# Performance work log

Measured on AMD Instinct MI355X. Metric: run time of the kernel, lower is better.

Reference implementation:

```python
import jax, jax.numpy as jnp
import numpy as np

# dims
N, E, C, HH, HEADS, A, V, D, AE, FH, MAXEL = 10000, 80000, 64, 128, 8, 32, 16, 64, 32, 128, 100
L, K = 2, 9  # lmax=2 -> (L+1)^2 = 9 steerable coefficients
EXPAND = jnp.array([0, 1, 1, 1, 2, 2, 2, 2, 2])          # coeff -> degree l
EXP1 = jnp.array([0, 0, 0, 1, 1, 1, 1, 1])                # coeffs 1..8 -> l-1
L_ONEHOT = jax.nn.one_hot(EXPAND, 3, dtype=jnp.float32)   # [9,3]
COUNTS = jnp.array([1 * C, 3 * C, 5 * C], dtype=jnp.float32)


def so3_linear(h, W, b):
    # per-degree linear (SO3_LinearV2): W [3,Cin,Cout], bias only on l=0
    out = jnp.einsum('nkc,kcd->nkd', h, W[EXPAND])
    return out.at[:, 0].add(b)


def enorm(h):
    # equivariant norm: per-node, per-degree RMS over (m, channels)
    sq = jnp.einsum('nkc,kl->nl', h * h, L_ONEHOT)        # [N,3] sum of squares per l
    scale = jax.lax.rsqrt(sq / COUNTS + 1e-6)             # [N,3]
    return h * scale[:, EXPAND][:, :, None]


def seg_softmax(logits, seg, n):
    m = jax.ops.segment_max(logits, seg, num_segments=n)
    m = jnp.where(jnp.isfinite(m), m, 0.0)
    e = jnp.exp(logits - m[seg])
    s = jax.ops.segment_sum(e, seg, num_segments=n)
    return e / (s[seg] + 1e-9)


def smooth_leaky_relu(z, a=0.2):
    return a * z + (1.0 - a) * z * jax.nn.sigmoid(z)


def setup_inputs():
    key = jax.random.key(0)
    ks = jax.random.split(key, 20)
    p = lambda i, sh, s=0.05: jax.random.normal(ks[i], sh, jnp.float32) * s
    return {
        'x': jax.random.normal(ks[0], (N, K, C), jnp.float32),
        'edge_distance': jax.random.uniform(ks[1], (E, D), dtype=jnp.float32),
        'rl_ij': jax.random.normal(ks[2], (E, K - 1), jnp.float32),
        'src_emb': p(3, (MAXEL, AE), 0.001),
        'tgt_emb': p(4, (MAXEL, AE), 0.001),
        'W1': p(5, (D + 2 * AE, 128)), 'b1': jnp.zeros((128,), jnp.float32),
        'W2': p(6, (128, 3 * 2 * C)), 'b2': jnp.zeros((3 * 2 * C,), jnp.float32),
        'W_conv1': p(7, (3, 2 * C, HH)),
        'W_m0': p(8, (2 * C, HEADS * A + HH + 2 * L * HH)),
        'ln_g': jnp.ones((A,), jnp.float32), 'ln_b': jnp.zeros((A,), jnp.float32),
        'alpha_dot': p(9, (HEADS, A), 0.2),
        'W_xj': p(10, (C, HH)),
        'W_conv2': p(11, (3, HH, HEADS * V)),
        'W_proj': p(12, (3, HEADS * V, C)), 'b_proj': jnp.zeros((C,), jnp.float32),
        'W_gate': p(13, (C, FH)), 'b_gate': jnp.zeros((FH,), jnp.float32),
        'W_ffn1': p(14, (3, C, FH)), 'b_ffn1': jnp.zeros((FH,), jnp.float32),
        'W_ffn2': p(15, (3, FH, C)), 'b_ffn2': jnp.zeros((C,), jnp.float32),
        'atomic_numbers': jax.random.randint(ks[16], (N,), 0, MAXEL),
        'edge_index': jax.random.randint(ks[17], (2, E), 0, N),
    }


def _block(x, edge_distance, rl_ij, src_emb, tgt_emb, W1, b1, W2, b2, W_conv1,
           W_m0, ln_g, ln_b, alpha_dot, W_xj, W_conv2, W_proj, b_proj,
           W_gate, b_gate, W_ffn1, b_ffn1, W_ffn2, b_ffn2,
           atomic_numbers, edge_index):
    src, tgt = edge_index[0], edge_index[1]
    # ---- attention branch (pre-norm) ----
    xn = enorm(x)
    xs, xt = xn[src], xn[tgt]                                    # [E,9,C] gathers
    x_edge = jnp.concatenate([xs, xt], axis=-1)                  # [E,9,2C]
    # radial function with source/target atom embeddings (use_m_share_rad)
    ef = jnp.concatenate([edge_distance, src_emb[atomic_numbers[src]],
                          tgt_emb[atomic_numbers[tgt]]], axis=-1)
    rad = jax.nn.silu(ef @ W1 + b1) @ W2 + b2                    # [E, 3*2C]
    rad = rad.reshape(E, 3, 2 * C)[:, EXPAND]                    # [E,9,2C]
    x_edge = x_edge * rad
    # so2_conv_1: per-degree linear + extra m0 scalar outputs
    msg = jnp.einsum('ekc,kcd->ekd', x_edge, W_conv1[EXPAND])    # [E,9,HH]
    extra = x_edge[:, 0] @ W_m0                                  # [E,896]
    alpha_f = extra[:, :HEADS * A].reshape(E, HEADS, A)
    g_scalar = extra[:, HEADS * A:HEADS * A + HH]                # [E,HH]
    gates = extra[:, HEADS * A + HH:].reshape(E, 2, L, HH)
    g_dir = jax.nn.sigmoid(gates[:, 0])[:, EXP1]                 # [E,8,HH]
    g_ten = jax.nn.sigmoid(gates[:, 1])[:, EXP1]                 # [E,8,HH]
    # GATA value activation: scalar silu + gated direction/tensor terms (l>=1)
    xj_proj = jnp.einsum('ekc,cd->ekd', xs, W_xj)                # [E,9,HH]
    val0 = jax.nn.silu(g_scalar)                                 # [E,HH]
    val_rest = msg[:, 1:] + rl_ij[:, :, None] * g_dir + xj_proj[:, 1:] * g_ten
    val = jnp.concatenate([val0[:, None], val_rest], axis=1)     # [E,9,HH]
    # so2_conv_2
    vout = jnp.einsum('ekd,kdh->ekh', val, W_conv2[EXPAND])      # [E,9,H*V]
    # attention weights
    mu = jnp.mean(alpha_f, axis=-1, keepdims=True)
    var = jnp.var(alpha_f, axis=-1, keepdims=True)
    an = (alpha_f - mu) * jax.lax.rsqrt(var + 1e-5) * ln_g + ln_b
    logits = jnp.einsum('eha,ha->eh', smooth_leaky_relu(an), alpha_dot)
    attn = seg_softmax(logits, tgt, N)                           # [E,HEADS]
    vout = vout.reshape(E, K, HEADS, V) * attn[:, None, :, None]
    node_out = jax.ops.segment_sum(vout.reshape(E, K, HEADS * V), tgt,
                                   num_segments=N)               # [N,9,H*V]
    x = x + so3_linear(node_out, W_proj, b_proj)
    # ---- FFN branch (pre-norm, separable S2-style gating) ----
    yn = enorm(x)
    g = yn[:, 0] @ W_gate + b_gate                               # [N,FH]
    h = so3_linear(yn, W_ffn1, b_ffn1)                           # [N,9,FH]
    h = jnp.concatenate([jax.nn.silu(g)[:, None],
                         h[:, 1:] * jax.nn.sigmoid(g)[:, None, :]], axis=1)
    return x + so3_linear(h, W_ffn2, b_ffn2)


def reference(x, edge_distance, rl_ij, src_emb, tgt_emb, W1, b1, W2, b2,
              W_conv1, W_m0, ln_g, ln_b, alpha_dot, W_xj, W_conv2, W_proj,
              b_proj, W_gate, b_gate, W_ffn1, b_ffn1, W_ffn2, b_ffn2,
              atomic_numbers, edge_index):
    return _block(x, edge_distance, rl_ij, src_emb, tgt_emb, W1, b1, W2, b2,
                  W_conv1, W_m0, ln_g, ln_b, alpha_dot, W_xj, W_conv2, W_proj,
                  b_proj, W_gate, b_gate, W_ffn1, b_ffn1, W_ffn2, b_ffn2,
                  atomic_numbers, edge_index)
```

## Files before the change

### kernel.cpp

```cpp
#include <hip/hip_runtime.h>

#define NN 10000
#define EE 80000

__device__ __forceinline__ float bf2f(unsigned short u) {
  return __uint_as_float(((unsigned)u) << 16);
}
__device__ __forceinline__ unsigned short f2bf(float f) {
  unsigned u = __float_as_uint(f);
  return (unsigned short)((u + 0x7FFFu + ((u >> 16) & 1u)) >> 16);
}
__device__ __forceinline__ float sigm(float x) { return 1.0f / (1.0f + __expf(-x)); }
__device__ __forceinline__ float siluf(float x) { return x * sigm(x); }

__device__ __forceinline__ float ld1(const void* p, long i, bool isf) {
  return isf ? ((const float*)p)[i] : bf2f(((const unsigned short*)p)[i]);
}
__device__ __forceinline__ void st1(void* p, long i, float v, bool isf) {
  if (isf) ((float*)p)[i] = v;
  else     ((unsigned short*)p)[i] = f2bf(v);
}
struct F8 { float v[8]; };
__device__ __forceinline__ F8 ld8(const void* p, long i, bool isf) {
  F8 r;
  if (isf) {
    const float* q = (const float*)p + i;
    float4 a = *(const float4*)q;
    float4 b = *(const float4*)(q + 4);
    r.v[0] = a.x; r.v[1] = a.y; r.v[2] = a.z; r.v[3] = a.w;
    r.v[4] = b.x; r.v[5] = b.y; r.v[6] = b.z; r.v[7] = b.w;
  } else {
    uint4 u = *(const uint4*)((const unsigned short*)p + i);
    r.v[0] = __uint_as_float(u.x << 16); r.v[1] = __uint_as_float(u.x & 0xFFFF0000u);
    r.v[2] = __uint_as_float(u.y << 16); r.v[3] = __uint_as_float(u.y & 0xFFFF0000u);
    r.v[4] = __uint_as_float(u.z << 16); r.v[5] = __uint_as_float(u.z & 0xFFFF0000u);
    r.v[6] = __uint_as_float(u.w << 16); r.v[7] = __uint_as_float(u.w & 0xFFFF0000u);
  }
  return r;
}
__device__ __forceinline__ void ld4v(const void* p, long i, bool isf, float o[4]) {
  if (isf) {
    float4 v = *(const float4*)((const float*)p + i);
    o[0] = v.x; o[1] = v.y; o[2] = v.z; o[3] = v.w;
  } else {
    uint2 u = *(const uint2*)((const unsigned short*)p + i);
    o[0] = bf2f((unsigned short)u.x); o[1] = bf2f((unsigned short)(u.x >> 16));
    o[2] = bf2f((unsigned short)u.y); o[3] = bf2f((unsigned short)(u.y >> 16));
  }
}
__device__ __forceinline__ void ldx4(const unsigned short* p, long i, float o[4]) {
  uint2 u = *(const uint2*)(p + i);
  o[0] = bf2f((unsigned short)u.x); o[1] = bf2f((unsigned short)(u.x >> 16));
  o[2] = bf2f((unsigned short)u.y); o[3] = bf2f((unsigned short)(u.y >> 16));
}
__device__ __forceinline__ void st4bf(unsigned short* dst, float a, float b,
                                      float c, float d) {
  uint2 u;
  u.x = (unsigned)f2bf(a) | ((unsigned)f2bf(b) << 16);
  u.y = (unsigned)f2bf(c) | ((unsigned)f2bf(d) << 16);
  *(uint2*)dst = u;
}
__device__ __forceinline__ float u8f(unsigned v) {
  return (float)(v & 0xFFu) * (1.f / 255.f);
}

typedef __attribute__((ext_vector_type(8))) short bf8v;
typedef __attribute__((ext_vector_type(4))) float f4v;
struct AF128 { bf8v a[4]; };
struct AF64  { bf8v a[2]; };
struct BF128 { bf8v b[4]; };
struct BF64  { bf8v b[2]; };

__device__ __forceinline__ AF128 load_af128(const unsigned short* sA, int pitch, int lane) {
  AF128 f;
  const unsigned short* p = sA + (lane & 15) * pitch + ((lane >> 4) << 3);
#pragma unroll
  for (int kb = 0; kb < 4; ++kb) f.a[kb] = *(const bf8v*)(p + kb * 32);
  return f;
}
__device__ __forceinline__ AF64 load_af64(const unsigned short* sA, int pitch, int lane) {
  AF64 f;
  const unsigned short* p = sA + (lane & 15) * pitch + ((lane >> 4) << 3);
#pragma unroll
  for (int kb = 0; kb < 2; ++kb) f.a[kb] = *(const bf8v*)(p + kb * 32);
  return f;
}
__device__ __forceinline__ BF128 load_b128(const unsigned short* Wt, int row0, int lane) {
  BF128 f;
  const unsigned short* p = Wt + (long)(row0 + (lane & 15)) * 128 + ((lane >> 4) << 3);
#pragma unroll
  for (int kb = 0; kb < 4; ++kb) f.b[kb] = *(const bf8v*)(p + kb * 32);
  return f;
}
__device__ __forceinline__ BF64 load_b64f(const unsigned short* Wt, int row0, int lane) {
  BF64 f;
  const unsigned short* p = Wt + (long)(row0 + (lane & 15)) * 64 + ((lane >> 4) << 3);
#pragma unroll
  for (int kb = 0; kb < 2; ++kb) f.b[kb] = *(const bf8v*)(p + kb * 32);
  return f;
}
__device__ __forceinline__ f4v mfma128f(const AF128& a, const BF128& w) {
  f4v acc = {0.f, 0.f, 0.f, 0.f};
#pragma unroll
  for (int kb = 0; kb < 4; ++kb)
    acc = __builtin_amdgcn_mfma_f32_16x16x32_bf16(a.a[kb], w.b[kb], acc, 0, 0, 0);
  return acc;
}
__device__ __forceinline__ f4v mfma64f(const AF64& a, const BF64& w) {
  f4v acc = {0.f, 0.f, 0.f, 0.f};
#pragma unroll
  for (int kb = 0; kb < 2; ++kb)
    acc = __builtin_amdgcn_mfma_f32_16x16x32_bf16(a.a[kb], w.b[kb], acc, 0, 0, 0);
  return acc;
}
__device__ __forceinline__ f4v mfma128w(const BF128& w, const AF128& x) {
  f4v acc = {0.f, 0.f, 0.f, 0.f};
#pragma unroll
  for (int kb = 0; kb < 4; ++kb)
    acc = __builtin_amdgcn_mfma_f32_16x16x32_bf16(w.b[kb], x.a[kb], acc, 0, 0, 0);
  return acc;
}
__device__ __forceinline__ f4v mfma64w(const BF64& w, const AF64& x) {
  f4v acc = {0.f, 0.f, 0.f, 0.f};
#pragma unroll
  for (int kb = 0; kb < 2; ++kb)
    acc = __builtin_amdgcn_mfma_f32_16x16x32_bf16(w.b[kb], x.a[kb], acc, 0, 0, 0);
  return acc;
}
__device__ __forceinline__ f4v mfma128(const AF128& f, const unsigned short* Wt,
                                       int row0, int lane) {
  return mfma128f(f, load_b128(Wt, row0, lane));
}
__device__ __forceinline__ f4v mfma64(const AF64& f, const unsigned short* Wt,
                                      int row0, int lane) {
  return mfma64f(f, load_b64f(Wt, row0, lane));
}
__device__ __forceinline__ void store8(unsigned short* dst, const unsigned short v[8]) {
  uint4 u;
  u.x = (unsigned)v[0] | ((unsigned)v[1] << 16);
  u.y = (unsigned)v[2] | ((unsigned)v[3] << 16);
  u.z = (unsigned)v[4] | ((unsigned)v[5] << 16);
  u.w = (unsigned)v[6] | ((unsigned)v[7] << 16);
  *(uint4*)dst = u;
}

#define OFF_W1 0
#define OFF_W2 16384
#define OFF_M0 65536
#define OFF_C1 180224
#define OFF_XJ 229376
#define OFF_C2 237568
#define OFF_PJ 286720
#define OFF_G  311296
#define OFF_F1 319488
#define OFF_F2 344064
#define WT_TOTAL 368640

#define WS_SBUF   1177280
#define WS_LOGB   1497280
#define WS_CURS   2777280
#define WS_PERM   2817280
#define WS_NOUT   3137280
#define WS_XN     49217280

__global__ __launch_bounds__(256) void k_repack(
    const void* __restrict__ W1, const void* __restrict__ W2,
    const void* __restrict__ W_m0, const void* __restrict__ W_conv1,
    const void* __restrict__ W_xj, const void* __restrict__ W_conv2,
    const void* __restrict__ W_proj, const void* __restrict__ W_gate,
    const void* __restrict__ W_ffn1, const void* __restrict__ W_ffn2,
    const void* __restrict__ ln_g, unsigned short* __restrict__ wt) {
  const bool isf = (((const unsigned*)ln_g)[0] == 0x3F800000u);
  int i = blockIdx.x * 256 + threadIdx.x;
  float v;
  if (i < 16384)       { int n = i >> 7, k = i & 127; v = ld1(W1, (long)k * 128 + n, isf); }
  else if (i < 65536)  { int j = i - 16384; int n = j >> 7, k = j & 127;
                         v = ld1(W2, (long)k * 384 + n, isf); }
  else if (i < 180224) { int j = i - 65536; int n = j >> 7, k = j & 127;
                         v = ld1(W_m0, (long)k * 896 + n, isf); }
  else if (i < 229376) { int j = i - 180224; int l = j >> 14, r = j & 16383;
                         int n = r >> 7, k = r & 127;
                         v = ld1(W_conv1, (long)(l * 128 + k) * 128 + n, isf); }
  else if (i < 237568) { int j = i - 229376; int n = j >> 6, k = j & 63;
                         v = ld1(W_xj, (long)k * 128 + n, isf); }
  else if (i < 286720) { int j = i - 237568; int l = j >> 14, r = j & 16383;
                         int n = r >> 7, k = r & 127;
                         v = ld1(W_conv2, (long)(l * 128 + k) * 128 + n, isf); }
  else if (i < 311296) { int j = i - 286720; int l = j >> 13, r = j & 8191;
                         int n = r >> 7, k = r & 127;
                         v = ld1(W_proj, (long)(l * 128 + k) * 64 + n, isf); }
  else if (i < 319488) { int j = i - 311296; int n = j >> 6, k = j & 63;
                         v = ld1(W_gate, (long)k * 128 + n, isf); }
  else if (i < 344064) { int j = i - 319488; int l = j >> 13, r = j & 8191;
                         int n = r >> 6, k = r & 63;
                         v = ld1(W_ffn1, (long)(l * 64 + k) * 128 + n, isf); }
  else                 { int j = i - 344064; int l = j >> 13, r = j & 8191;
                         int n = r >> 7, k = r & 127;
                         v = ld1(W_ffn2, (long)(l * 128 + k) * 64 + n, isf); }
  wt[i] = f2bf(v);
}

__global__ __launch_bounds__(256) void k_scales(const void* __restrict__ x,
                                                const void* __restrict__ ln_g,
                                                unsigned short* __restrict__ xn) {
  const bool isf = (((const unsigned*)ln_g)[0] == 0x3F800000u);
  const int n = blockIdx.x * 4 + (threadIdx.x >> 6);
  const int c = threadIdx.x & 63;
  long xb = (long)n * 576;
  float v[9];
#pragma unroll
  for (int k = 0; k < 9; ++k) v[k] = ld1(x, xb + k * 64 + c, isf);
  float q0 = v[0] * v[0], q1 = 0.f, q2 = 0.f;
#pragma unroll
  for (int k = 1; k < 4; ++k) q1 += v[k] * v[k];
#pragma unroll
  for (int k = 4; k < 9; ++k) q2 += v[k] * v[k];
#pragma unroll
  for (int off = 32; off > 0; off >>= 1) {
    q0 += __shfl_xor(q0, off); q1 += __shfl_xor(q1, off); q2 += __shfl_xor(q2, off);
  }
  float s0 = rsqrtf(q0 * (1.f / 64.f)  + 1e-6f);
  float s1 = rsqrtf(q1 * (1.f / 192.f) + 1e-6f);
  float s2 = rsqrtf(q2 * (1.f / 320.f) + 1e-6f);
  xn[xb + c] = f2bf(v[0] * s0);
#pragma unroll
  for (int k = 1; k < 4; ++k) xn[xb + k * 64 + c] = f2bf(v[k] * s1);
#pragma unroll
  for (int k = 4; k < 9; ++k) xn[xb + k * 64 + c] = f2bf(v[k] * s2);
}

__global__ void k_init0(float* __restrict__ p) {
  int i = blockIdx.x * 256 + threadIdx.x;
  if (i < 80000) p[i] = 0.f;
}
__global__ void k_initn(float4* __restrict__ p) {
  int i = blockIdx.x * 256 + threadIdx.x;
  p[i] = make_float4(0.f, 0.f, 0.f, 0.f);
}
__global__ void k_zc(int* __restrict__ c) {
  int i = blockIdx.x * 256 + threadIdx.x;
  if (i < NN) c[i] = 0;
}
__global__ void k_hist(const int* __restrict__ edge_index, int* __restrict__ cnt) {
  int e = blockIdx.x * 256 + threadIdx.x;
  if (e < EE) atomicAdd(&cnt[edge_index[EE + e]], 1);
}
__global__ __launch_bounds__(256) void k_prefix(int* __restrict__ cur) {
  __shared__ int part[256], off0[256];
  const int th = threadIdx.x;
  int cnt[40]; int s = 0;
#pragma unroll 1
  for (int i = 0; i < 40; ++i) {
    int n = th * 40 + i;
    cnt[i] = (n < NN) ? cur[n] : 0;
    s += cnt[i];
  }
  part[th] = s;
  __syncthreads();
  if (th == 0) {
    int acc = 0;
    for (int i = 0; i < 256; ++i) { off0[i] = acc; acc += part[i]; }
  }
  __syncthreads();
  int acc = off0[th];
#pragma unroll 1
  for (int i = 0; i < 40; ++i) {
    int n = th * 40 + i;
    if (n < NN) { cur[n] = acc; acc += cnt[i]; }
  }
}
__global__ void k_scatter(const int* __restrict__ edge_index, int* __restrict__ cur,
                          int* __restrict__ perm) {
  int e = blockIdx.x * 256 + threadIdx.x;
  if (e < EE) {
    int tg = edge_index[EE + e];
    int pos = atomicAdd(&cur[tg], 1);
    perm[pos] = e;
  }
}

__global__ __launch_bounds__(256) void k_logits_e(
    const unsigned short* __restrict__ xn, const void* __restrict__ dist,
    const void* __restrict__ src_emb, const void* __restrict__ tgt_emb,
    const void* __restrict__ b1, const void* __restrict__ b2,
    const void* __restrict__ ln_g, const void* __restrict__ ln_b,
    const void* __restrict__ alpha_dot,
    const int* __restrict__ an, const int* __restrict__ edge_index,
    const unsigned short* __restrict__ wt,
    unsigned short* __restrict__ logitsb, float* __restrict__ sbuf) {
  const bool isf = (((const unsigned*)ln_g)[0] == 0x3F800000u);
  __shared__ int s_src[32], s_tgt[32], s_as[32], s_at[32];
  __shared__ __align__(16) unsigned short sA[32 * 136];
  __shared__ __align__(16) unsigned short sA2[32 * 136];
  __shared__ __align__(16) unsigned short sFB[32 * 264];

  const int t = threadIdx.x;
  int bid = blockIdx.x;
  int x8 = bid & 7, i8 = bid >> 3;
  int wg = (x8 < 4 ? x8 * 313 : 1252 + (x8 - 4) * 312) + i8;
  const int e0 = wg * 32;
  const int lane = t & 63, wave = t >> 6, lm = lane & 15, lq = lane >> 4;

  if (t < 32) {
    int eid = e0 + t;
    int s = edge_index[eid], g = edge_index[EE + eid];
    s_src[t] = s; s_tgt[t] = g;
    s_as[t] = an[s]; s_at[t] = an[g];
  }
  __syncthreads();
#pragma unroll
  for (int ee = 0; ee < 2; ++ee) {
    int e = ee * 16 + (t >> 4), c0 = (t & 15) * 8;
    int eid = e0 + e;
    F8 vv;
    if (c0 < 64)      vv = ld8(dist, (long)eid * 64 + c0, isf);
    else if (c0 < 96) vv = ld8(src_emb, (long)s_as[e] * 32 + (c0 - 64), isf);
    else              vv = ld8(tgt_emb, (long)s_at[e] * 32 + (c0 - 96), isf);
    unsigned short v8[8];
#pragma unroll
    for (int j = 0; j < 8; ++j) v8[j] = f2bf(vv.v[j]);
    store8(&sA[e * 136 + c0], v8);
  }
  __syncthreads();
  {
    AF128 fa0 = load_af128(sA, 136, lane);
    AF128 fa1 = load_af128(sA + 16 * 136, 136, lane);
#pragma unroll
    for (int i = 0; i < 2; ++i) {
      int nt = wave + 4 * i;
      BF128 w = load_b128(wt + OFF_W1, nt * 16, lane);
      f4v d0 = mfma128w(w, fa0);
      f4v d1 = mfma128w(w, fa1);
      int hc = nt * 16 + lq * 4;
      float bb[4]; ld4v(b1, hc, isf, bb);
      st4bf(&sA2[lm * 136 + hc],
            siluf(d0[0] + bb[0]), siluf(d0[1] + bb[1]),
            siluf(d0[2] + bb[2]), siluf(d0[3] + bb[3]));
      st4bf(&sA2[(16 + lm) * 136 + hc],
            siluf(d1[0] + bb[0]), siluf(d1[1] + bb[1]),
            siluf(d1[2] + bb[2]), siluf(d1[3] + bb[3]));
    }
  }
  __syncthreads();
  {
    AF128 fh0 = load_af128(sA2, 136, lane);
    AF128 fh1 = load_af128(sA2 + 16 * 136, 136, lane);
#pragma unroll
    for (int i = 0; i < 2; ++i) {
      int nt = wave + 4 * i;
      BF128 w = load_b128(wt + OFF_W2, nt * 16, lane);
      f4v dd[2] = { mfma128w(w, fh0), mfma128w(w, fh1) };
      int rc = nt * 16 + lq * 4;
      float bb[4]; ld4v(b2, rc, isf, bb);
#pragma unroll
      for (int g = 0; g < 2; ++g) {
        int m = g * 16 + lm;
        float xv[4];
        if (rc < 64) ldx4(xn, (long)s_src[m] * 576 + rc, xv);
        else         ldx4(xn, (long)s_tgt[m] * 576 + (rc - 64), xv);
        st4bf(&sA[m * 136 + rc],
              (dd[g][0] + bb[0]) * xv[0], (dd[g][1] + bb[1]) * xv[1],
              (dd[g][2] + bb[2]) * xv[2], (dd[g][3] + bb[3]) * xv[3]);
      }
    }
  }
  __syncthreads();
  {
    AF128 fe0 = load_af128(sA, 136, lane);
    AF128 fe1 = load_af128(sA + 16 * 136, 136, lane);
#pragma unroll
    for (int i = 0; i < 4; ++i) {
      int nt = wave + 4 * i;
      BF128 w = load_b128(wt + OFF_M0, nt * 16, lane);
      f4v d0 = mfma128w(w, fe0);
      f4v d1 = mfma128w(w, fe1);
      int ac = nt * 16 + lq * 4;
      st4bf(&sFB[lm * 264 + ac], d0[0], d0[1], d0[2], d0[3]);
      st4bf(&sFB[(16 + lm) * 264 + ac], d1[0], d1[1], d1[2], d1[3]);
    }
  }
  __syncthreads();
  {
    int e = t >> 3, h = t & 7;
    const unsigned short* ap = &sFB[e * 264 + h * 32];
    float m1 = 0.f, m2 = 0.f;
#pragma unroll
    for (int a = 0; a < 32; ++a) { float v = bf2f(ap[a]); m1 += v; m2 += v * v; }
    float mu = m1 * (1.f / 32.f);
    float var = m2 * (1.f / 32.f) - mu * mu;
    float rstd = rsqrtf(fmaxf(var, 0.f) + 1e-5f);
    float acc = 0.f;
#pragma unroll
    for (int a = 0; a < 32; ++a) {
      float anv = (bf2f(ap[a]) - mu) * rstd * ld1(ln_g, a, isf) + ld1(ln_b, a, isf);
      float z = 0.2f * anv + 0.8f * anv * sigm(anv);
      acc = fmaf(z, ld1(alpha_dot, (long)h * 32 + a, isf), acc);
    }
    unsigned short lb = f2bf(acc);
    logitsb[(long)(e0 + e) * 8 + h] = lb;
    atomicAdd(&sbuf[s_tgt[e] * 8 + h], __expf(bf2f(lb)));
  }
}

__global__ __launch_bounds__(256, 3) void k_chain_e(
    const unsigned short* __restrict__ xn,
    const void* __restrict__ dist, const void* __restrict__ rl_ij,
    const void* __restrict__ src_emb, const void* __restrict__ tgt_emb,
    const void* __restrict__ b1, const void* __restrict__ b2,
    const void* __restrict__ ln_g,
    const int* __restrict__ an, const int* __restrict__ edge_index,
    const int* __restrict__ perm,
    const unsigned short* __restrict__ wt,
    const unsigned short* __restrict__ logitsb,
    const float* __restrict__ sbuf, float* __restrict__ node_out) {
  const bool isf = (((const unsigned*)ln_g)[0] == 0x3F800000u);
  __shared__ int s_src[16], s_tgt[16], s_as[16], s_at[16], s_eid[16];
  __shared__ float s_aw[16][8], s_rl[16][8];
  __shared__ __align__(16) unsigned short sPOOL[128 * 136];
  __shared__ __align__(16) unsigned short sRAD[16 * 264];
  __shared__ __align__(8) unsigned char sGd[16 * 264];
  __shared__ __align__(8) unsigned char sGt[16 * 264];

  const int t = threadIdx.x;
  int bid = blockIdx.x;
  const int e0b = ((bid & 7) * 625 + (bid >> 3)) * 16;
  const int lane = t & 63, wave = t >> 6, lm = lane & 15, lq = lane >> 4;

  if (t < 16) {
    int eid = perm[e0b + t];
    int s = edge_index[eid], g = edge_index[EE + eid];
    s_eid[t] = eid;
    s_src[t] = s; s_tgt[t] = g;
    s_as[t] = an[s]; s_at[t] = an[g];
  }
  __syncthreads();

  const int kA = 1 + wave * 2, kB = kA + 1;
  const int lA = (kA < 4) ? 1 : 2, lB = (kB < 4) ? 1 : 2;
  const int gA = lA - 1, gB = lB - 1;
  const long sbase = (long)s_src[lm] * 576 + (lq << 3);
  const long tbase = (long)s_tgt[lm] * 576 + (lq << 3);
  bf8v ggA[4], ggB[4];
  ggA[0] = *(const bf8v*)(xn + sbase + kA * 64);
  ggA[1] = *(const bf8v*)(xn + sbase + kA * 64 + 32);
  ggA[2] = *(const bf8v*)(xn + tbase + kA * 64);
  ggA[3] = *(const bf8v*)(xn + tbase + kA * 64 + 32);
  ggB[0] = *(const bf8v*)(xn + sbase + kB * 64);
  ggB[1] = *(const bf8v*)(xn + sbase + kB * 64 + 32);
  ggB[2] = *(const bf8v*)(xn + tbase + kB * 64);
  ggB[3] = *(const bf8v*)(xn + tbase + kB * 64 + 32);

  if (t < 128) {
    int e = t >> 3, h = t & 7;
    int eid = s_eid[e];
    float ss = sbuf[s_tgt[e] * 8 + h];
    s_aw[e][h] = __expf(bf2f(logitsb[(long)eid * 8 + h])) / (ss + 1e-9f);
    s_rl[e][h] = ld1(rl_ij, (long)eid * 8 + h, isf);
  }
  {
    int e = t >> 4, c0 = (t & 15) * 8;
    int eid = s_eid[e];
    F8 vv;
    if (c0 < 64)      vv = ld8(dist, (long)eid * 64 + c0, isf);
    else if (c0 < 96) vv = ld8(src_emb, (long)s_as[e] * 32 + (c0 - 64), isf);
    else              vv = ld8(tgt_emb, (long)s_at[e] * 32 + (c0 - 96), isf);
    unsigned short v8[8];
#pragma unroll
    for (int j = 0; j < 8; ++j) v8[j] = f2bf(vv.v[j]);
    store8(&sPOOL[e * 136 + c0], v8);
  }
  __syncthreads();
  {
    AF128 fa = load_af128(sPOOL, 136, lane);
#pragma unroll
    for (int i = 0; i < 2; ++i) {
      int nt = wave + 4 * i;
      BF128 w = load_b128(wt + OFF_W1, nt * 16, lane);
      f4v d = mfma128w(w, fa);
      int hc = nt * 16 + lq * 4;
      float bb[4]; ld4v(b1, hc, isf, bb);
      st4bf(&sPOOL[(16 + lm) * 136 + hc],
            siluf(d[0] + bb[0]), siluf(d[1] + bb[1]),
            siluf(d[2] + bb[2]), siluf(d[3] + bb[3]));
    }
  }
  __syncthreads();
  {
    AF128 fh = load_af128(sPOOL + 16 * 136, 136, lane);
#pragma unroll
    for (int i = 0; i < 6; ++i) {
      int nt = wave + 4 * i;
      BF128 w = load_b128(wt + OFF_W2, nt * 16, lane);
      f4v d = mfma128w(w, fh);
      int rc = nt * 16 + lq * 4;
      float bb[4]; ld4v(b2, rc, isf, bb);
      if (i < 2) {
        float xv[4];
        if (rc < 64) ldx4(xn, (long)s_src[lm] * 576 + rc, xv);
        else         ldx4(xn, (long)s_tgt[lm] * 576 + (rc - 64), xv);
        st4bf(&sPOOL[lm * 136 + rc],
              (d[0] + bb[0]) * xv[0], (d[1] + bb[1]) * xv[1],
              (d[2] + bb[2]) * xv[2], (d[3] + bb[3]) * xv[3]);
      } else {
        st4bf(&sRAD[lm * 264 + (rc - 128)],
              d[0] + bb[0], d[1] + bb[1], d[2] + bb[2], d[3] + bb[3]);
      }
    }
  }
  __syncthreads();
  {
    AF128 fe = load_af128(sPOOL, 136, lane);
#pragma unroll
    for (int i = 0; i < 10; ++i) {
      int nt = wave + 4 * i;
      BF128 w = load_b128(wt + OFF_M0 + 256 * 128, nt * 16, lane);
      f4v d = mfma128w(w, fe);
      int oc = nt * 16 + lq * 4;
      if (i < 2) {
        st4bf(&sPOOL[(16 + lm) * 136 + oc],
              siluf(d[0]), siluf(d[1]), siluf(d[2]), siluf(d[3]));
      } else {
        int c = oc - 128;
        unsigned q0 = __float2uint_rn(sigm(d[0]) * 255.f);
        unsigned q1 = __float2uint_rn(sigm(d[1]) * 255.f);
        unsigned q2 = __float2uint_rn(sigm(d[2]) * 255.f);
        unsigned q3 = __float2uint_rn(sigm(d[3]) * 255.f);
        unsigned pk = q0 | (q1 << 8) | (q2 << 16) | (q3 << 24);
        if (c < 256) *(unsigned*)&sGd[lm * 264 + c]         = pk;
        else         *(unsigned*)&sGt[lm * 264 + (c - 256)] = pk;
      }
    }
  }
  __syncthreads();
  {
    AF128 fv = load_af128(sPOOL + 16 * 136, 136, lane);
#pragma unroll
    for (int i = 0; i < 2; ++i) {
      int nt = wave + 4 * i;
      f4v d = mfma128(fv, wt + OFF_C2, nt * 16, lane);
      int col = nt * 16 + lm, h = col >> 4;
      float acc = 0.f; int cur = s_tgt[lq * 4];
#pragma unroll
      for (int r = 0; r < 4; ++r) {
        int m = lq * 4 + r;
        int tg = s_tgt[m];
        float v = s_aw[m][h] * d[r];
        if (tg != cur) {
          atomicAdd(&node_out[(long)cur * 1152 + col], acc);
          acc = 0.f; cur = tg;
        }
        acc += v;
      }
      atomicAdd(&node_out[(long)cur * 1152 + col], acc);
    }
  }
  __syncthreads();

  {
    const int er = lm;
    const float rlA = s_rl[er][kA - 1], rlB = s_rl[er][kB - 1];
    AF128 fmA, fmB; AF64 fxA, fxB;
    fxA.a[0] = ggA[0]; fxA.a[1] = ggA[1];
    fxB.a[0] = ggB[0]; fxB.a[1] = ggB[1];
    const unsigned short* rpA = sRAD + er * 264 + gA * 128 + (lq << 3);
    const unsigned short* rpB = sRAD + er * 264 + gB * 128 + (lq << 3);
#pragma unroll
    for (int kb = 0; kb < 4; ++kb) {
      bf8v rvA = *(const bf8v*)(rpA + kb * 32);
      bf8v rvB = *(const bf8v*)(rpB + kb * 32);
      bf8v oA, oB;
#pragma unroll
      for (int j = 0; j < 8; ++j) {
        oA[j] = (short)f2bf(bf2f((unsigned short)ggA[kb][j]) *
                            bf2f((unsigned short)rvA[j]));
        oB[j] = (short)f2bf(bf2f((unsigned short)ggB[kb][j]) *
                            bf2f((unsigned short)rvB[j]));
      }
      fmA.a[kb] = oA; fmB.a[kb] = oB;
    }
    unsigned short* vbA = sPOOL + (wave * 32) * 136;
    unsigned short* vbB = vbA + 16 * 136;
#pragma unroll
    for (int mt = 0; mt < 8; ++mt) {
      BF128 w1A = load_b128(wt + OFF_C1 + lA * 16384, mt * 16, lane);
      BF128 w1B;
      if (lB == lA) w1B = w1A;
      else          w1B = load_b128(wt + OFF_C1 + lB * 16384, mt * 16, lane);
      BF64 wx = load_b64f(wt + OFF_XJ, mt * 16, lane);
      f4v dmA = mfma128w(w1A, fmA);
      f4v dmB = mfma128w(w1B, fmB);
      f4v dxA = mfma64w(wx, fxA);
      f4v dxB = mfma64w(wx, fxB);
      int d0 = mt * 16 + lq * 4;
      unsigned gdA = *(const unsigned*)&sGd[er * 264 + (gA << 7) + d0];
      unsigned gtA = *(const unsigned*)&sGt[er * 264 + (gA << 7) + d0];
      unsigned gdB, gtB;
      if (gB == gA) { gdB = gdA; gtB = gtA; }
      else {
        gdB = *(const unsigned*)&sGd[er * 264 + (gB << 7) + d0];
        gtB = *(const unsigned*)&sGt[er * 264 + (gB << 7) + d0];
      }
      st4bf(&vbA[er * 136 + d0],
            dmA[0] + rlA * u8f(gdA)       + dxA[0] * u8f(gtA),
            dmA[1] + rlA * u8f(gdA >> 8)  + dxA[1] * u8f(gtA >> 8),
            dmA[2] + rlA * u8f(gdA >> 16) + dxA[2] * u8f(gtA >> 16),
            dmA[3] + rlA * u8f(gdA >> 24) + dxA[3] * u8f(gtA >> 24));
      st4bf(&vbB[er * 136 + d0],
            dmB[0] + rlB * u8f(gdB)       + dxB[0] * u8f(gtB),
            dmB[1] + rlB * u8f(gdB >> 8)  + dxB[1] * u8f(gtB >> 8),
            dmB[2] + rlB * u8f(gdB >> 16) + dxB[2] * u8f(gtB >> 16),
            dmB[3] + rlB * u8f(gdB >> 24) + dxB[3] * u8f(gtB >> 24));
    }
    AF128 fvA = load_af128(vbA, 136, lane);
    AF128 fvB = load_af128(vbB, 136, lane);
#pragma unroll
    for (int nt = 0; nt < 8; ++nt) {
      const int col = nt * 16 + lm;
      BF128 w2A = load_b128(wt + OFF_C2 + lA * 16384, nt * 16, lane);
      BF128 w2B;
      if (lB == lA) w2B = w2A;
      else          w2B = load_b128(wt + OFF_C2 + lB * 16384, nt * 16, lane);
      f4v dA = mfma128f(fvA, w2A);
      f4v dB = mfma128f(fvB, w2B);
      float accA = 0.f, accB = 0.f; int cur = s_tgt[lq * 4];
#pragma unroll
      for (int r = 0; r < 4; ++r) {
        int m = lq * 4 + r;
        int tg = s_tgt[m];
        if (tg != cur) {
          atomicAdd(&node_out[(long)cur * 1152 + kA * 128 + col], accA);
          atomicAdd(&node_out[(long)cur * 1152 + kB * 128 + col], accB);
          accA = 0.f; accB = 0.f; cur = tg;
        }
        accA += s_aw[m][nt] * dA[r];
        accB += s_aw[m][nt] * dB[r];
      }
      atomicAdd(&node_out[(long)cur * 1152 + kA * 128 + col], accA);
      atomicAdd(&node_out[(long)cur * 1152 + kB * 128 + col], accB);
    }
  }
}

__global__ __launch_bounds__(256) void k_epi_mfma(
    const void* __restrict__ x,
    const void* __restrict__ b_proj, const void* __restrict__ b_gate,
    const void* __restrict__ b_ffn2, const void* __restrict__ ln_g,
    const unsigned short* __restrict__ wt,
    const float* __restrict__ node_out, void* __restrict__ out) {
  const bool isf = (((const unsigned*)ln_g)[0] == 0x3F800000u);
  __shared__ __align__(16) char POOL[96768];
  unsigned short* sIN = (unsigned short*)POOL;
  float* sXN = (float*)(POOL + 39168);
  unsigned short* sYN = (unsigned short*)(POOL + 76032);
  unsigned short* sH  = sIN;
  __shared__ float s_sgf[16][128];
  __shared__ float s_nsc[16][3];

  const int t = threadIdx.x;
  int bid = blockIdx.x;
  int x8 = bid & 7, i8 = bid >> 3;
  int wg = (x8 < 1) ? i8 : (79 + (x8 - 1) * 78 + i8);
  const int n0 = wg * 16;
  const int lane = t & 63, wave = t >> 6, lm = lane & 15, lq = lane >> 4;

#pragma unroll
  for (int it = 0; it < 9; ++it) {
    int u = t + it * 256;
    int row = u >> 4, c0 = (u & 15) * 8;
    int k = row >> 4, n = row & 15;
    const float4* q = (const float4*)&node_out[(long)(n0 + n) * 1152 + k * 128 + c0];
    float4 a = q[0], b = q[1];
    unsigned short v8[8] = { f2bf(a.x), f2bf(a.y), f2bf(a.z), f2bf(a.w),
                             f2bf(b.x), f2bf(b.y), f2bf(b.z), f2bf(b.w) };
    store8(&sIN[row * 136 + c0], v8);
  }
  __syncthreads();
  for (int tid = wave; tid < 36; tid += 4) {
    int mt = tid >> 2, ntile = tid & 3;
    int l = (mt == 0) ? 0 : ((mt < 4) ? 1 : 2);
    AF128 fa = load_af128(sIN + mt * 16 * 136, 136, lane);
    f4v d = mfma128(fa, wt + OFF_PJ + l * 8192, ntile * 16, lane);
    int col = ntile * 16 + lm;
#pragma unroll
    for (int r = 0; r < 4; ++r) {
      int row = mt * 16 + lq * 4 + r;
      int n = row & 15, k = mt;
      float v = d[r] + ld1(x, (long)(n0 + n) * 576 + k * 64 + col, isf);
      if (k == 0) v += ld1(b_proj, col, isf);
      sXN[row * 64 + col] = v;
    }
  }
  __syncthreads();
  {
    int n = t >> 4, c4 = (t & 15) * 4;
    float q0 = 0.f, q1 = 0.f, q2 = 0.f;
#pragma unroll
    for (int k = 0; k < 9; ++k)
#pragma unroll
      for (int j = 0; j < 4; ++j) {
        float v = sXN[(k * 16 + n) * 64 + c4 + j];
        float vv = v * v;
        if (k == 0) q0 += vv; else if (k < 4) q1 += vv; else q2 += vv;
      }
#pragma unroll
    for (int off = 8; off > 0; off >>= 1) {
      q0 += __shfl_xor(q0, off); q1 += __shfl_xor(q1, off); q2 += __shfl_xor(q2, off);
    }
    if ((t & 15) == 0) {
      s_nsc[n][0] = rsqrtf(q0 * (1.f / 64.f)  + 1e-6f);
      s_nsc[n][1] = rsqrtf(q1 * (1.f / 192.f) + 1e-6f);
      s_nsc[n][2] = rsqrtf(q2 * (1.f / 320.f) + 1e-6f);
    }
  }
  __syncthreads();
#pragma unroll
  for (int it = 0; it < 5; ++it) {
    int u = t + it * 256;
    if (u < 1152) {
      int row = u >> 3, c0 = (u & 7) * 8;
      int k = row >> 4, n = row & 15;
      int l = (k == 0) ? 0 : ((k < 4) ? 1 : 2);
      float sc = s_nsc[n][l];
      unsigned short v8[8];
#pragma unroll
      for (int j = 0; j < 8; ++j) v8[j] = f2bf(sXN[row * 64 + c0 + j] * sc);
      store8(&sYN[row * 72 + c0], v8);
    }
  }
  __syncthreads();
  {
    AF64 fg = load_af64(sYN, 72, lane);
    for (int nt = wave; nt < 8; nt += 4) {
      f4v d = mfma64(fg, wt + OFF_G, nt * 16, lane);
      int col = nt * 16 + lm;
#pragma unroll
      for (int r = 0; r < 4; ++r) {
        int n = lq * 4 + r;
        float gv = d[r] + ld1(b_gate, col, isf);
        float sg = sigm(gv);
        s_sgf[n][col] = sg;
        sH[n * 136 + col] = f2bf(gv * sg);
      }
    }
  }
  __syncthreads();
  for (int tid = wave; tid < 64; tid += 4) {
    int mt = 1 + (tid >> 3), ntile = tid & 7;
    int l = (mt < 4) ? 1 : 2;
    AF64 fy = load_af64(sYN + mt * 16 * 72, 72, lane);
    f4v d = mfma64(fy, wt + OFF_F1 + l * 8192, ntile * 16, lane);
    int col = ntile * 16 + lm;
#pragma unroll
    for (int r = 0; r < 4; ++r) {
      int row = mt * 16 + lq * 4 + r;
      int n = row & 15;
      sH[row * 136 + col] = f2bf(d[r] * s_sgf[n][col]);
    }
  }
  __syncthreads();
  for (int tid = wave; tid < 36; tid += 4) {
    int mt = tid >> 2, ntile = tid & 3;
    int l = (mt == 0) ? 0 : ((mt < 4) ? 1 : 2);
    AF128 fh = load_af128(sH + mt * 16 * 136, 136, lane);
    f4v d = mfma128(fh, wt + OFF_F2 + l * 8192, ntile * 16, lane);
    int col = ntile * 16 + lm;
#pragma unroll
    for (int r = 0; r < 4; ++r) {
      int row = mt * 16 + lq * 4 + r;
      int n = row & 15, k = mt;
      float v = sXN[row * 64 + col] + d[r];
      if (k == 0) v += ld1(b_ffn2, col, isf);
      st1(out, (long)(n0 + n) * 576 + k * 64 + col, v, isf);
    }
  }
}

extern "C" void kernel_launch(void* const* d_in, const int* in_sizes, int n_in,
                              void* d_out, int out_size, void* d_ws, size_t ws_size,
                              hipStream_t stream) {
  (void)in_sizes; (void)n_in; (void)out_size; (void)ws_size;
  char* ws = (char*)d_ws;
  unsigned short* wt   = (unsigned short*)ws;
  float*    sbuf       = (float*)(ws + WS_SBUF);
  unsigned short* logb = (unsigned short*)(ws + WS_LOGB);
  int*      cursor     = (int*)(ws + WS_CURS);
  int*      perm       = (int*)(ws + WS_PERM);
  float*    node_out   = (float*)(ws + WS_NOUT);
  unsigned short* xnb  = (unsigned short*)(ws + WS_XN);
  const int* an        = (const int*)d_in[24];
  const int* ei        = (const int*)d_in[25];

  k_repack<<<WT_TOTAL / 256, 256, 0, stream>>>(
      d_in[5], d_in[7], d_in[10], d_in[9], d_in[14], d_in[15],
      d_in[16], d_in[18], d_in[20], d_in[22], d_in[11], wt);
  k_scales<<<NN / 4, 256, 0, stream>>>(d_in[0], d_in[11], xnb);
  k_init0<<<313, 256, 0, stream>>>(sbuf);
  k_initn<<<11250, 256, 0, stream>>>((float4*)node_out);
  k_zc<<<40, 256, 0, stream>>>(cursor);
  k_hist<<<(EE + 255) / 256, 256, 0, stream>>>(ei, cursor);
  k_prefix<<<1, 256, 0, stream>>>(cursor);
  k_scatter<<<(EE + 255) / 256, 256, 0, stream>>>(ei, cursor, perm);
  k_logits_e<<<EE / 32, 256, 0, stream>>>(
      xnb, d_in[1], d_in[3], d_in[4], d_in[6], d_in[8],
      d_in[11], d_in[12], d_in[13], an, ei, wt, logb, sbuf);
  k_chain_e<<<EE / 16, 256, 0, stream>>>(
      xnb, d_in[1], d_in[2], d_in[3], d_in[4], d_in[6], d_in[8], d_in[11],
      an, ei, perm, wt, logb, sbuf, node_out);
  k_epi_mfma<<<NN / 16, 256, 0, stream>>>(
      d_in[0], d_in[17], d_in[19], d_in[23], d_in[11], wt, node_out, d_out);
}
```

Measured before the change: 864.7 us.

## Fuse logits into edge kernel and replace atomic scatter with CSR gather

Merges the logits kernel into the edge-chain kernel so the radial MLP and feature products are computed once per edge instead of twice. Each edge now writes its unweighted value output as bf16 in target-sorted order. The epilogue gathers those rows through the CSR offsets and applies the softmax weights there, which removes the float atomics and the zeroing of node_out. The cost is a large bf16 per-edge buffer that is written and then read back. There is also a fixed per-block cap of 384 edges for the attention weights, and a block with more incoming edges would read outside that buffer.

```diff
diff --git a/kernel.cpp b/kernel.cpp
--- a/kernel.cpp
+++ b/kernel.cpp
@@ -160,8 +160,8 @@
 #define WS_LOGB   1497280
 #define WS_CURS   2777280
 #define WS_PERM   2817280
-#define WS_NOUT   3137280
-#define WS_XN     49217280
+#define WS_VOUT   3137280
+#define WS_XN     187457280
 
 __global__ __launch_bounds__(256) void k_repack(
     const void* __restrict__ W1, const void* __restrict__ W2,
@@ -233,10 +233,6 @@
   int i = blockIdx.x * 256 + threadIdx.x;
   if (i < 80000) p[i] = 0.f;
 }
-__global__ void k_initn(float4* __restrict__ p) {
-  int i = blockIdx.x * 256 + threadIdx.x;
-  p[i] = make_float4(0.f, 0.f, 0.f, 0.f);
-}
 __global__ void k_zc(int* __restrict__ c) {
   int i = blockIdx.x * 256 + threadIdx.x;
   if (i < NN) c[i] = 0;
@@ -279,155 +275,33 @@
   }
 }
 
-__global__ __launch_bounds__(256) void k_logits_e(
-    const unsigned short* __restrict__ xn, const void* __restrict__ dist,
+__global__ __launch_bounds__(256, 3) void k_edge(
+    const unsigned short* __restrict__ xn,
+    const void* __restrict__ dist, const void* __restrict__ rl_ij,
     const void* __restrict__ src_emb, const void* __restrict__ tgt_emb,
     const void* __restrict__ b1, const void* __restrict__ b2,
     const void* __restrict__ ln_g, const void* __restrict__ ln_b,
     const void* __restrict__ alpha_dot,
     const int* __restrict__ an, const int* __restrict__ edge_index,
-    const unsigned short* __restrict__ wt,
-    unsigned short* __restrict__ logitsb, float* __restrict__ sbuf) {
-  const bool isf = (((const unsigned*)ln_g)[0] == 0x3F800000u);
-  __shared__ int s_src[32], s_tgt[32], s_as[32], s_at[32];
-  __shared__ __align__(16) unsigned short sA[32 * 136];
-  __shared__ __align__(16) unsigned short sA2[32 * 136];
-  __shared__ __align__(16) unsigned short sFB[32 * 264];
-
-  const int t = threadIdx.x;
-  int bid = blockIdx.x;
-  int x8 = bid & 7, i8 = bid >> 3;
-  int wg = (x8 < 4 ? x8 * 313 : 1252 + (x8 - 4) * 312) + i8;
-  const int e0 = wg * 32;
-  const int lane = t & 63, wave = t >> 6, lm = lane & 15, lq = lane >> 4;
-
-  if (t < 32) {
-    int eid = e0 + t;
-    int s = edge_index[eid], g = edge_index[EE + eid];
-    s_src[t] = s; s_tgt[t] = g;
-    s_as[t] = an[s]; s_at[t] = an[g];
-  }
-  __syncthreads();
-#pragma unroll
-  for (int ee = 0; ee < 2; ++ee) {
-    int e = ee * 16 + (t >> 4), c0 = (t & 15) * 8;
-    int eid = e0 + e;
-    F8 vv;
-    if (c0 < 64)      vv = ld8(dist, (long)eid * 64 + c0, isf);
-    else if (c0 < 96) vv = ld8(src_emb, (long)s_as[e] * 32 + (c0 - 64), isf);
-    else              vv = ld8(tgt_emb, (long)s_at[e] * 32 + (c0 - 96), isf);
-    unsigned short v8[8];
-#pragma unroll
-    for (int j = 0; j < 8; ++j) v8[j] = f2bf(vv.v[j]);
-    store8(&sA[e * 136 + c0], v8);
-  }
-  __syncthreads();
-  {
-    AF128 fa0 = load_af128(sA, 136, lane);
-    AF128 fa1 = load_af128(sA + 16 * 136, 136, lane);
-#pragma unroll
-    for (int i = 0; i < 2; ++i) {
-      int nt = wave + 4 * i;
-      BF128 w = load_b128(wt + OFF_W1, nt * 16, lane);
-      f4v d0 = mfma128w(w, fa0);
-      f4v d1 = mfma128w(w, fa1);
-      int hc = nt * 16 + lq * 4;
-      float bb[4]; ld4v(b1, hc, isf, bb);
-      st4bf(&sA2[lm * 136 + hc],
-            siluf(d0[0] + bb[0]), siluf(d0[1] + bb[1]),
-            siluf(d0[2] + bb[2]), siluf(d0[3] + bb[3]));
-      st4bf(&sA2[(16 + lm) * 136 + hc],
-            siluf(d1[0] + bb[0]), siluf(d1[1] + bb[1]),
-            siluf(d1[2] + bb[2]), siluf(d1[3] + bb[3]));
-    }
-  }
-  __syncthreads();
-  {
-    AF128 fh0 = load_af128(sA2, 136, lane);
-    AF128 fh1 = load_af128(sA2 + 16 * 136, 136, lane);
-#pragma unroll
-    for (int i = 0; i < 2; ++i) {
-      int nt = wave + 4 * i;
-      BF128 w = load_b128(wt + OFF_W2, nt * 16, lane);
-      f4v dd[2] = { mfma128w(w, fh0), mfma128w(w, fh1) };
-      int rc = nt * 16 + lq * 4;
-      float bb[4]; ld4v(b2, rc, isf, bb);
-#pragma unroll
-      for (int g = 0; g < 2; ++g) {
-        int m = g * 16 + lm;
-        float xv[4];
-        if (rc < 64) ldx4(xn, (long)s_src[m] * 576 + rc, xv);
-        else         ldx4(xn, (long)s_tgt[m] * 576 + (rc - 64), xv);
-        st4bf(&sA[m * 136 + rc],
-              (dd[g][0] + bb[0]) * xv[0], (dd[g][1] + bb[1]) * xv[1],
-              (dd[g][2] + bb[2]) * xv[2], (dd[g][3] + bb[3]) * xv[3]);
-      }
-    }
-  }
-  __syncthreads();
-  {
-    AF128 fe0 = load_af128(sA, 136, lane);
-    AF128 fe1 = load_af128(sA + 16 * 136, 136, lane);
-#pragma unroll
-    for (int i = 0; i < 4; ++i) {
-      int nt = wave + 4 * i;
-      BF128 w = load_b128(wt + OFF_M0, nt * 16, lane);
-      f4v d0 = mfma128w(w, fe0);
-      f4v d1 = mfma128w(w, fe1);
-      int ac = nt * 16 + lq * 4;
-      st4bf(&sFB[lm * 264 + ac], d0[0], d0[1], d0[2], d0[3]);
-      st4bf(&sFB[(16 + lm) * 264 + ac], d1[0], d1[1], d1[2], d1[3]);
-    }
-  }
-  __syncthreads();
-  {
-    int e = t >> 3, h = t & 7;
-    const unsigned short* ap = &sFB[e * 264 + h * 32];
-    float m1 = 0.f, m2 = 0.f;
-#pragma unroll
-    for (int a = 0; a < 32; ++a) { float v = bf2f(ap[a]); m1 += v; m2 += v * v; }
-    float mu = m1 * (1.f / 32.f);
-    float var = m2 * (1.f / 32.f) - mu * mu;
-    float rstd = rsqrtf(fmaxf(var, 0.f) + 1e-5f);
-    float acc = 0.f;
-#pragma unroll
-    for (int a = 0; a < 32; ++a) {
-      float anv = (bf2f(ap[a]) - mu) * rstd * ld1(ln_g, a, isf) + ld1(ln_b, a, isf);
-      float z = 0.2f * anv + 0.8f * anv * sigm(anv);
-      acc = fmaf(z, ld1(alpha_dot, (long)h * 32 + a, isf), acc);
-    }
-    unsigned short lb = f2bf(acc);
-    logitsb[(long)(e0 + e) * 8 + h] = lb;
-    atomicAdd(&sbuf[s_tgt[e] * 8 + h], __expf(bf2f(lb)));
-  }
-}
-
-__global__ __launch_bounds__(256, 3) void k_chain_e(
-    const unsigned short* __restrict__ xn,
-    const void* __restrict__ dist, const void* __restrict__ rl_ij,
-    const void* __restrict__ src_emb, const void* __restrict__ tgt_emb,
-    const void* __restrict__ b1, const void* __restrict__ b2,
-    const void* __restrict__ ln_g,
-    const int* __restrict__ an, const int* __restrict__ edge_index,
     const int* __restrict__ perm,
     const unsigned short* __restrict__ wt,
-    const unsigned short* __restrict__ logitsb,
-    const float* __restrict__ sbuf, float* __restrict__ node_out) {
+    unsigned short* __restrict__ logitsb, float* __restrict__ sbuf,
+    unsigned short* __restrict__ vout) {
   const bool isf = (((const unsigned*)ln_g)[0] == 0x3F800000u);
   __shared__ int s_src[16], s_tgt[16], s_as[16], s_at[16], s_eid[16];
-  __shared__ float s_aw[16][8], s_rl[16][8];
+  __shared__ float s_rl[16][8];
   __shared__ __align__(16) unsigned short sPOOL[128 * 136];
   __shared__ __align__(16) unsigned short sRAD[16 * 264];
   __shared__ __align__(8) unsigned char sGd[16 * 264];
   __shared__ __align__(8) unsigned char sGt[16 * 264];
+  unsigned short* sFB = sPOOL + 64 * 136;
 
   const int t = threadIdx.x;
-  int bid = blockIdx.x;
-  const int e0b = ((bid & 7) * 625 + (bid >> 3)) * 16;
+  const int pb = blockIdx.x * 16;
   const int lane = t & 63, wave = t >> 6, lm = lane & 15, lq = lane >> 4;
 
   if (t < 16) {
-    int eid = perm[e0b + t];
+    int eid = perm[pb + t];
     int s = edge_index[eid], g = edge_index[EE + eid];
     s_eid[t] = eid;
     s_src[t] = s; s_tgt[t] = g;
@@ -452,10 +326,7 @@
 
   if (t < 128) {
     int e = t >> 3, h = t & 7;
-    int eid = s_eid[e];
-    float ss = sbuf[s_tgt[e] * 8 + h];
-    s_aw[e][h] = __expf(bf2f(logitsb[(long)eid * 8 + h])) / (ss + 1e-9f);
-    s_rl[e][h] = ld1(rl_ij, (long)eid * 8 + h, isf);
+    s_rl[e][h] = ld1(rl_ij, (long)s_eid[e] * 8 + h, isf);
   }
   {
     int e = t >> 4, c0 = (t & 15) * 8;
@@ -508,6 +379,38 @@
     }
   }
   __syncthreads();
+  {
+    AF128 fe = load_af128(sPOOL, 136, lane);
+#pragma unroll
+    for (int i = 0; i < 4; ++i) {
+      int nt = wave + 4 * i;
+      BF128 w = load_b128(wt + OFF_M0, nt * 16, lane);
+      f4v d = mfma128w(w, fe);
+      int ac = nt * 16 + lq * 4;
+      st4bf(&sFB[lm * 264 + ac], d[0], d[1], d[2], d[3]);
+    }
+  }
+  __syncthreads();
+  if (t < 128) {
+    int e = t >> 3, h = t & 7;
+    const unsigned short* ap = &sFB[e * 264 + h * 32];
+    float m1 = 0.f, m2 = 0.f;
+#pragma unroll
+    for (int a = 0; a < 32; ++a) { float v = bf2f(ap[a]); m1 += v; m2 += v * v; }
+    float mu = m1 * (1.f / 32.f);
+    float var = m2 * (1.f / 32.f) - mu * mu;
+    float rstd = rsqrtf(fmaxf(var, 0.f) + 1e-5f);
+    float acc = 0.f;
+#pragma unroll
+    for (int a = 0; a < 32; ++a) {
+      float anv = (bf2f(ap[a]) - mu) * rstd * ld1(ln_g, a, isf) + ld1(ln_b, a, isf);
+      float z = 0.2f * anv + 0.8f * anv * sigm(anv);
+      acc = fmaf(z, ld1(alpha_dot, (long)h * 32 + a, isf), acc);
+    }
+    unsigned short lb = f2bf(acc);
+    logitsb[(long)(pb + e) * 8 + h] = lb;
+    atomicAdd(&sbuf[s_tgt[e] * 8 + h], __expf(bf2f(lb)));
+  }
   {
     AF128 fe = load_af128(sPOOL, 136, lane);
 #pragma unroll
@@ -537,21 +440,10 @@
 #pragma unroll
     for (int i = 0; i < 2; ++i) {
       int nt = wave + 4 * i;
-      f4v d = mfma128(fv, wt + OFF_C2, nt * 16, lane);
-      int col = nt * 16 + lm, h = col >> 4;
-      float acc = 0.f; int cur = s_tgt[lq * 4];
-#pragma unroll
-      for (int r = 0; r < 4; ++r) {
-        int m = lq * 4 + r;
-        int tg = s_tgt[m];
-        float v = s_aw[m][h] * d[r];
-        if (tg != cur) {
-          atomicAdd(&node_out[(long)cur * 1152 + col], acc);
-          acc = 0.f; cur = tg;
-        }
-        acc += v;
-      }
-      atomicAdd(&node_out[(long)cur * 1152 + col], acc);
+      BF128 w = load_b128(wt + OFF_C2, nt * 16, lane);
+      f4v d = mfma128w(w, fv);
+      int d0 = nt * 16 + lq * 4;
+      st4bf(vout + (long)(pb + lm) * 1152 + d0, d[0], d[1], d[2], d[3]);
     }
   }
   __syncthreads();
@@ -613,40 +505,31 @@
     }
     AF128 fvA = load_af128(vbA, 136, lane);
     AF128 fvB = load_af128(vbB, 136, lane);
+    unsigned short* vrow = vout + (long)(pb + lm) * 1152;
 #pragma unroll
     for (int nt = 0; nt < 8; ++nt) {
-      const int col = nt * 16 + lm;
       BF128 w2A = load_b128(wt + OFF_C2 + lA * 16384, nt * 16, lane);
       BF128 w2B;
       if (lB == lA) w2B = w2A;
       else          w2B = load_b128(wt + OFF_C2 + lB * 16384, nt * 16, lane);
-      f4v dA = mfma128f(fvA, w2A);
-      f4v dB = mfma128f(fvB, w2B);
-      float accA = 0.f, accB = 0.f; int cur = s_tgt[lq * 4];
-#pragma unroll
-      for (int r = 0; r < 4; ++r) {
-        int m = lq * 4 + r;
-        int tg = s_tgt[m];
-        if (tg != cur) {
-          atomicAdd(&node_out[(long)cur * 1152 + kA * 128 + col], accA);
-          atomicAdd(&node_out[(long)cur * 1152 + kB * 128 + col], accB);
-          accA = 0.f; accB = 0.f; cur = tg;
-        }
-        accA += s_aw[m][nt] * dA[r];
-        accB += s_aw[m][nt] * dB[r];
-      }
-      atomicAdd(&node_out[(long)cur * 1152 + kA * 128 + col], accA);
-      atomicAdd(&node_out[(long)cur * 1152 + kB * 128 + col], accB);
-    }
-  }
-}
-
+      f4v dA = mfma128w(w2A, fvA);
+      f4v dB = mfma128w(w2B, fvB);
+      int d0 = nt * 16 + lq * 4;
+      st4bf(vrow + kA * 128 + d0, dA[0], dA[1], dA[2], dA[3]);
+      st4bf(vrow + kB * 128 + d0, dB[0], dB[1], dB[2], dB[3]);
+    }
+  }
+}
+
+#define MAXE 384
 __global__ __launch_bounds__(256) void k_epi_mfma(
     const void* __restrict__ x,
     const void* __restrict__ b_proj, const void* __restrict__ b_gate,
     const void* __restrict__ b_ffn2, const void* __restrict__ ln_g,
     const unsigned short* __restrict__ wt,
-    const float* __restrict__ node_out, void* __restrict__ out) {
+    const int* __restrict__ cursor,
+    const unsigned short* __restrict__ logitsb, const float* __restrict__ sbuf,
+    const unsigned short* __restrict__ vout, void* __restrict__ out) {
   const bool isf = (((const unsigned*)ln_g)[0] == 0x3F800000u);
   __shared__ __align__(16) char POOL[96768];
   unsigned short* sIN = (unsigned short*)POOL;
@@ -655,24 +538,52 @@
   unsigned short* sH  = sIN;
   __shared__ float s_sgf[16][128];
   __shared__ float s_nsc[16][3];
+  __shared__ int s_off[17];
+  __shared__ float s_aw[MAXE][8];
 
   const int t = threadIdx.x;
-  int bid = blockIdx.x;
-  int x8 = bid & 7, i8 = bid >> 3;
-  int wg = (x8 < 1) ? i8 : (79 + (x8 - 1) * 78 + i8);
-  const int n0 = wg * 16;
+  const int n0 = blockIdx.x * 16;
   const int lane = t & 63, wave = t >> 6, lm = lane & 15, lq = lane >> 4;
 
-#pragma unroll
-  for (int it = 0; it < 9; ++it) {
-    int u = t + it * 256;
-    int row = u >> 4, c0 = (u & 15) * 8;
-    int k = row >> 4, n = row & 15;
-    const float4* q = (const float4*)&node_out[(long)(n0 + n) * 1152 + k * 128 + c0];
-    float4 a = q[0], b = q[1];
-    unsigned short v8[8] = { f2bf(a.x), f2bf(a.y), f2bf(a.z), f2bf(a.w),
-                             f2bf(b.x), f2bf(b.y), f2bf(b.z), f2bf(b.w) };
-    store8(&sIN[row * 136 + c0], v8);
+  if (t < 17) {
+    int n = n0 + t - 1;
+    s_off[t] = (n < 0) ? 0 : cursor[n];
+  }
+  __syncthreads();
+  const int p0 = s_off[0];
+  for (int n = 0; n < 16; ++n) {
+    int a = s_off[n] - p0, b = s_off[n + 1] - p0;
+    for (int i = t; i < (b - a) * 8; i += 256) {
+      int pl = a + (i >> 3), h = i & 7;
+      if (pl < MAXE)
+        s_aw[pl][h] = __expf(bf2f(logitsb[(long)(p0 + pl) * 8 + h])) /
+                      (sbuf[(n0 + n) * 8 + h] + 1e-9f);
+    }
+  }
+  __syncthreads();
+  {
+    for (int n = 0; n < 16; ++n) {
+      int a = s_off[n] - p0, b = s_off[n + 1] - p0;
+      float acc[5] = {0.f, 0.f, 0.f, 0.f, 0.f};
+      for (int pl = a; pl < b; ++pl) {
+        const unsigned short* vr = vout + (long)(p0 + pl) * 1152;
+        const float* awr = s_aw[pl];
+#pragma unroll
+        for (int j = 0; j < 5; ++j) {
+          int idx = t + j * 256;
+          if (j < 4 || t < 128)
+            acc[j] += bf2f(vr[idx]) * awr[(idx & 127) >> 4];
+        }
+      }
+#pragma unroll
+      for (int j = 0; j < 5; ++j) {
+        int idx = t + j * 256;
+        if (j < 4 || t < 128) {
+          int k = idx >> 7, col = idx & 127;
+          sIN[(k * 16 + n) * 136 + col] = f2bf(acc[j]);
+        }
+      }
+    }
   }
   __syncthreads();
   for (int tid = wave; tid < 36; tid += 4) {
@@ -785,7 +696,7 @@
   unsigned short* logb = (unsigned short*)(ws + WS_LOGB);
   int*      cursor     = (int*)(ws + WS_CURS);
   int*      perm       = (int*)(ws + WS_PERM);
-  float*    node_out   = (float*)(ws + WS_NOUT);
+  unsigned short* voutb= (unsigned short*)(ws + WS_VOUT);
   unsigned short* xnb  = (unsigned short*)(ws + WS_XN);
   const int* an        = (const int*)d_in[24];
   const int* ei        = (const int*)d_in[25];
@@ -795,17 +706,14 @@
       d_in[16], d_in[18], d_in[20], d_in[22], d_in[11], wt);
   k_scales<<<NN / 4, 256, 0, stream>>>(d_in[0], d_in[11], xnb);
   k_init0<<<313, 256, 0, stream>>>(sbuf);
-  k_initn<<<11250, 256, 0, stream>>>((float4*)node_out);
   k_zc<<<40, 256, 0, stream>>>(cursor);
   k_hist<<<(EE + 255) / 256, 256, 0, stream>>>(ei, cursor);
   k_prefix<<<1, 256, 0, stream>>>(cursor);
   k_scatter<<<(EE + 255) / 256, 256, 0, stream>>>(ei, cursor, perm);
-  k_logits_e<<<EE / 32, 256, 0, stream>>>(
-      xnb, d_in[1], d_in[3], d_in[4], d_in[6], d_in[8],
-      d_in[11], d_in[12], d_in[13], an, ei, wt, logb, sbuf);
-  k_chain_e<<<EE / 16, 256, 0, stream>>>(
-      xnb, d_in[1], d_in[2], d_in[3], d_in[4], d_in[6], d_in[8], d_in[11],
-      an, ei, perm, wt, logb, sbuf, node_out);
+  k_edge<<<EE / 16, 256, 0, stream>>>(
+      xnb, d_in[1], d_in[2], d_in[3], d_in[4], d_in[6], d_in[8],
+      d_in[11], d_in[12], d_in[13], an, ei, perm, wt, logb, sbuf, voutb);
   k_epi_mfma<<<NN / 16, 256, 0, stream>>>(
-      d_in[0], d_in[17], d_in[19], d_in[23], d_in[11], wt, node_out, d_out);
-}
+      d_in[0], d_in[17], d_in[19], d_in[23], d_in[11], wt,
+      cursor, logb, sbuf, voutb, d_out);
+}
```

Result: slower. 1.164 ms (+34.6%).
